# Kernel optimization log

Measured on AMD Instinct MI355X. Metric: run time of the kernel, lower is better.

Reference implementation:

```python
import jax, jax.numpy as jnp
import numpy as np

GRID = np.array([128, 128, 128], dtype=np.int32)
CENTER = np.array([0.0, 0.0, 0.0], dtype=np.float32)
SIZE = np.array([200.0, 200.0, 200.0], dtype=np.float32)
KERNEL_WIDTH = 3.0
TOF_BIN = 1.0
TOF_SIGMA2 = 100.0
N_SAMPLES = 64  # samples per LOR
N_LORS = 100000


def _ray_points_weights(lors):
    # lors: [N,7] = (x1,y1,z1, x2,y2,z2, tof)
    p1, p2, tof = lors[:, :3], lors[:, 3:6], lors[:, 6]
    u = (jnp.arange(N_SAMPLES, dtype=lors.dtype) + 0.5) / N_SAMPLES  # [S]
    pts = p1[:, None, :] + u[None, :, None] * (p2 - p1)[:, None, :]  # [N,S,3]
    L = jnp.linalg.norm(p2 - p1, axis=-1)  # [N]
    d = (u[None, :] - 0.5) * L[:, None]    # signed distance from LOR midpoint [N,S]
    tc = (tof * TOF_BIN)[:, None]          # TOF-estimated annihilation offset
    gauss = jnp.exp(-0.5 * (d - tc) ** 2 / TOF_SIGMA2)
    w = gauss * (L / N_SAMPLES)[:, None] * KERNEL_WIDTH  # [N,S]
    return pts, w


def _trilinear_corners(pts, grid, center, size):
    g = jnp.asarray(np.asarray(grid, np.int32))
    gf = g.astype(pts.dtype)
    c = jnp.asarray(np.asarray(center, np.float32), pts.dtype)
    s = jnp.asarray(np.asarray(size, np.float32), pts.dtype)
    vox = (pts - (c - s / 2)) / (s / gf) - 0.5  # continuous voxel coords [N,S,3]
    i0 = jnp.floor(vox).astype(jnp.int32)
    f = vox - i0.astype(pts.dtype)
    corners = []
    for dx in (0, 1):
        for dy in (0, 1):
            for dz in (0, 1):
                off = jnp.array([dx, dy, dz], jnp.int32)
                ii = i0 + off
                wxyz = jnp.where(off == 1, f, 1 - f)  # [N,S,3]
                w = wxyz[..., 0] * wxyz[..., 1] * wxyz[..., 2]
                inb = jnp.all((ii >= 0) & (ii < g), axis=-1)
                iic = jnp.clip(ii, 0, g - 1)
                corners.append((iic, jnp.where(inb, w, jnp.zeros_like(w))))
    return corners


def projection(lors, image, grid, center, size):
    pts, w = _ray_points_weights(lors)
    vals = jnp.zeros(w.shape, w.dtype)
    for ii, cw in _trilinear_corners(pts, grid, center, size):
        vals = vals + cw * image[ii[..., 0], ii[..., 1], ii[..., 2]]
    return jnp.sum(vals * w, axis=1)  # [N]


def backprojection(lors, lor_values, grid, center, size, dtype):
    pts, w = _ray_points_weights(lors)
    contrib = lor_values[:, None] * w  # [N,S]
    g = tuple(int(x) for x in np.asarray(grid))
    strides = (g[1] * g[2], g[2], 1)
    flat = jnp.zeros(g[0] * g[1] * g[2], dtype)
    for ii, cw in _trilinear_corners(pts, grid, center, size):
        idx = ii[..., 0] * strides[0] + ii[..., 1] * strides[1] + ii[..., 2]
        flat = flat.at[idx.ravel()].add((contrib * cw).ravel())
    return flat.reshape(g)


def setup_inputs() -> dict:
    key = jax.random.key(0)
    k_img, k_eff, kx, ky, kz = jax.random.split(key, 5)
    shape = tuple(int(x) for x in GRID)
    image = jax.random.uniform(k_img, shape, dtype=jnp.float32)
    efficiency_map = jax.random.uniform(k_eff, shape, dtype=jnp.float32) + 0.5

    def make_lors(k):
        k1, k2 = jax.random.split(k)
        ends = jax.random.uniform(k1, (6, N_LORS), minval=-100.0, maxval=100.0)
        tof = jax.random.uniform(k2, (1, N_LORS), minval=-30.0, maxval=30.0)
        return jnp.concatenate([ends, tof], axis=0).astype(jnp.float32)  # [7,N]

    return {
        "image": image,
        "efficiency_map": efficiency_map,
        "xlors": make_lors(kx),
        "ylors": make_lors(ky),
        "zlors": make_lors(kz),
    }


def reference(image, efficiency_map, xlors, ylors, zlors):
    imgz = jnp.transpose(image)             # reverse axes, as tf.transpose
    imgx = jnp.transpose(imgz, (2, 0, 1))
    imgy = jnp.transpose(imgz, (1, 0, 2))
    effmap = jnp.transpose(efficiency_map)
    xl, yl, zl = xlors.T, ylors.T, zlors.T  # [N,7]

    # z-view
    pz = projection(zl, imgz, GRID, CENTER, SIZE)
    bpz = backprojection(zl, pz, GRID, CENTER, SIZE, image.dtype)

    # x-view: permute axes [0,2,1]
    gx, cx, sx = GRID[[0, 2, 1]], CENTER[[0, 2, 1]], SIZE[[0, 2, 1]]
    px = projection(xl, imgx, gx, cx, sx)
    bpx = backprojection(xl, px, gx, cx, sx, image.dtype)
    bpxt = jnp.transpose(bpx, (1, 2, 0))

    # y-view: permute axes [1,2,0]
    gy, cy, sy = GRID[[1, 2, 0]], CENTER[[1, 2, 0]], SIZE[[1, 2, 0]]
    py = projection(yl, imgy, gy, cy, sy)
    bpy = backprojection(yl, py, gy, cy, sy, image.dtype)
    bpyt = jnp.transpose(bpy, (1, 0, 2))

    result = imgz / effmap * (bpxt + bpyt + bpz)
    return jnp.transpose(result)
```

## Files before the change

### kernel.cpp

```cpp
#include <hip/hip_runtime.h>

#define NLOR 100000
#define NDL  300000
#define NS   64
#define G    128
#define NVOX (G*G*G)
#define EPS_A 0.05f
#define W_MIN 1.5e-4f
#define NBKT   256
#define NSLICE 16
#define HALO_N 9537
#define ACC17  4913
#define MAX_SLOTS 1024
#define REC_CAP 19200000u
#define QSCALE     32768.0f
#define INV_QSCALE (1.0f/32768.0f)

typedef unsigned int u32;
typedef unsigned long long u64;

#define O_COUNTS  0ull
#define O_OFF     32768ull
#define O_CURSOR  65536ull
#define O_SLOTOFF 98304ull
#define O_SLOT2Q  102400ull
#define O_RECS    131072ull
#define O_COPIES  (O_RECS + (u64)REC_CAP * 8ull)
#define WS_NEED   (O_COPIES + (u64)MAX_SLOTS * HALO_N * 4ull)

__device__ __forceinline__ void atomAddF32(float* p, float v) { unsafeAtomicAdd(p, v); }

struct Samp { float w, fA, fB, fC; int iA, iB, iC; };

__device__ __forceinline__ Samp sample_abc(const float* __restrict__ lp,
                                           int lor, int dir, int lane)
{
    const float p10 = lp[0 * NLOR + lor];
    const float p11 = lp[1 * NLOR + lor];
    const float p12 = lp[2 * NLOR + lor];
    const float d0  = lp[3 * NLOR + lor] - p10;
    const float d1  = lp[4 * NLOR + lor] - p11;
    const float d2  = lp[5 * NLOR + lor] - p12;
    const float tof = lp[6 * NLOR + lor];

    const float L = sqrtf(d0 * d0 + d1 * d1 + d2 * d2);
    const float u = ((float)lane + 0.5f) * (1.0f / NS);
    const float dd = (u - 0.5f) * L - tof;
    const float w = __expf(dd * dd * (-0.5f / 100.0f)) * L * (3.0f / NS);

    const float inv_vs = 1.0f / 1.5625f;
    const float v0 = (p10 + u * d0 + 100.0f) * inv_vs - 0.5f;
    const float v1 = (p11 + u * d1 + 100.0f) * inv_vs - 0.5f;
    const float v2 = (p12 + u * d2 + 100.0f) * inv_vs - 0.5f;

    const float f0 = floorf(v0), f1 = floorf(v1), f2 = floorf(v2);
    const int i0 = (int)f0, i1 = (int)f1, i2 = (int)f2;
    const float g0 = v0 - f0, g1 = v1 - f1, g2 = v2 - f2;

    Samp s; s.w = w;
    if (dir == 0)      { s.iA = i0; s.fA = g0; s.iB = i2; s.fB = g2; s.iC = i1; s.fC = g1; }
    else if (dir == 1) { s.iA = i2; s.fA = g2; s.iB = i0; s.fB = g0; s.iC = i1; s.fC = g1; }
    else               { s.iA = i2; s.fA = g2; s.iB = i1; s.fB = g1; s.iC = i0; s.fC = g0; }
    return s;
}

__device__ __forceinline__ int bucket_of(const Samp& s) {
    const int qA = (s.iA < 0 ? 0 : s.iA) >> 4;
    const int qB = (s.iB < 0 ? 0 : s.iB) >> 4;
    const int qC = (s.iC < 0 ? 0 : s.iC) >> 5;
    return (qA << 5) | (qB << 2) | qC;
}

__device__ __forceinline__ u64 encode_rec(const Samp& s, float sc) {
    const u32 qfA = min((int)(s.fA * 512.0f + 0.5f), 511);
    const u32 qfB = min((int)(s.fB * 512.0f + 0.5f), 511);
    const u32 qfC = min((int)(s.fC * 512.0f + 0.5f), 511);
    const u32 s13 = (__float_as_uint(sc) + 0x40000u) >> 19;
    return (u64)qfA | ((u64)qfB << 9) | ((u64)qfC << 18)
         | ((u64)(u32)(s.iA + 1) << 27) | ((u64)(u32)(s.iB + 1) << 35)
         | ((u64)(u32)(s.iC + 1) << 43) | ((u64)s13 << 51);
}

struct RunInfo { bool leader; int runlen; int ldr; };

__device__ __forceinline__ RunInfo run_detect(bool act, int q, int lane) {
    RunInfo r;
    const u64 act_mask = __ballot(act);
    const int qup = __shfl_up(q, 1, 64);
    r.leader = act && (lane == 0 || !((act_mask >> (lane - 1)) & 1ull) || qup != q);
    const u64 lead_mask = __ballot(r.leader);
    r.runlen = 0;
    if (r.leader) {
        const u64 stop_mask = (~act_mask) | lead_mask;
        const u64 gt = (lane == 63) ? 0ull : (stop_mask >> (lane + 1));
        const int e = gt ? (lane + 1 + (__ffsll((unsigned long long)gt) - 1)) : 64;
        r.runlen = e - lane;
    }
    r.ldr = 0;
    if (act) {
        const u64 below_eq = lead_mask &
            ((lane == 63) ? ~0ull : ((1ull << (lane + 1)) - 1ull));
        r.ldr = 63 - __clzll((unsigned long long)below_eq);
    }
    return r;
}

__global__ __launch_bounds__(256) void count_kernel(
    const float* __restrict__ xl, const float* __restrict__ yl, const float* __restrict__ zl,
    u32* __restrict__ counts)
{
    __shared__ u32 h[NBKT];
    const int tid = (int)threadIdx.x;
    h[tid] = 0;
    __syncthreads();
    const int wid = tid >> 6, lane = tid & 63;
    const int slice = (int)blockIdx.x & (NSLICE - 1);

    for (int dl = (int)blockIdx.x * 4 + wid; dl < NDL; dl += 8192) {
        const int dir = dl < NLOR ? 0 : (dl < 2 * NLOR ? 1 : 2);
        const int lor = dl - dir * NLOR;
        const float* lp = dir == 0 ? xl : (dir == 1 ? yl : zl);
        const Samp s = sample_abc(lp, lor, dir, lane);
        const bool act_w = (s.w >= W_MIN);
        const int q = bucket_of(s);
        const RunInfo r = run_detect(act_w, q, lane);
        if (r.leader) atomicAdd(&h[q], (u32)r.runlen);
    }
    __syncthreads();
    if (h[tid]) atomicAdd(&counts[tid * NSLICE + slice], h[tid]);
}

__global__ __launch_bounds__(1024) void scan_kernel(
    const u32* __restrict__ counts, u32* __restrict__ off, u32* __restrict__ cursor,
    u32* __restrict__ slot_off, u32* __restrict__ slot2q)
{
    __shared__ u32 part[1024];
    __shared__ u32 sl[256];
    const int t = (int)threadIdx.x;
    u32 c[4], ssum = 0;
    #pragma unroll
    for (int k = 0; k < 4; ++k) { c[k] = counts[t * 4 + k]; ssum += c[k]; }
    part[t] = ssum;
    __syncthreads();
    for (int ofs = 1; ofs < 1024; ofs <<= 1) {
        u32 v = (t >= ofs) ? part[t - ofs] : 0u;
        __syncthreads();
        part[t] += v;
        __syncthreads();
    }
    u32 run = (t == 0) ? 0u : part[t - 1];
    #pragma unroll
    for (int k = 0; k < 4; ++k) { off[t * 4 + k] = run; cursor[t * 4 + k] = run; run += c[k]; }
    if (t == 1023) off[4096] = part[1023];
    __syncthreads();

    if (t < 256) {
        const u32 len = part[t * 4 + 3] - (t ? part[t * 4 - 1] : 0u);
        const u32 total = part[1023];
        u32 target = (total + 699u) / 700u;
        if (target == 0) target = 1;
        u32 slots = (len + target - 1u) / target;
        slots = slots < 1u ? 1u : (slots > 64u ? 64u : slots);
        sl[t] = slots;
    }
    __syncthreads();
    for (int ofs = 1; ofs < 256; ofs <<= 1) {
        u32 v = (t >= ofs && t < 256) ? sl[t - ofs] : 0u;
        __syncthreads();
        if (t < 256) sl[t] += v;
        __syncthreads();
    }
    if (t < 256) {
        const u32 base = t ? sl[t - 1] : 0u;
        const u32 n = sl[t] - base;
        slot_off[t] = base;
        for (u32 k = 0; k < n; ++k) slot2q[base + k] = (u32)t;
        if (t == 255) slot_off[256] = sl[255];
    }
}

__global__ __launch_bounds__(256) void projscat_kernel(
    const float* __restrict__ img,
    const float* __restrict__ xl, const float* __restrict__ yl, const float* __restrict__ zl,
    const u32* __restrict__ off, u32* __restrict__ cursor, u64* __restrict__ recs)
{
    const int tid = (int)threadIdx.x;
    const int wid = tid >> 6, lane = tid & 63;
    const int slice = (int)blockIdx.x & (NSLICE - 1);

    for (int dl = (int)blockIdx.x * 4 + wid; dl < NDL; dl += 8192) {
        const int dir = dl < NLOR ? 0 : (dl < 2 * NLOR ? 1 : 2);
        const int lor = dl - dir * NLOR;
        const float* lp = dir == 0 ? xl : (dir == 1 ? yl : zl);
        const Samp s = sample_abc(lp, lor, dir, lane);

        float val = 0.0f;
        if (s.w >= W_MIN) {
            const float wA1 = s.fA, wA0 = 1.0f - s.fA;
            const float wB1 = s.fB, wB0 = 1.0f - s.fB;
            const float wC1 = s.fC, wC0 = 1.0f - s.fC;
            #pragma unroll
            for (int c = 0; c < 8; ++c) {
                const int oA = (c >> 2) & 1, oB = (c >> 1) & 1, oC = c & 1;
                const int A = s.iA + oA, B = s.iB + oB, C = s.iC + oC;
                const bool ok = ((unsigned)A < 128u) & ((unsigned)B < 128u) & ((unsigned)C < 128u);
                const int Ac = min(max(A, 0), 127), Bc = min(max(B, 0), 127), Cc = min(max(C, 0), 127);
                const float cw = ok ? (oA ? wA1 : wA0) * (oB ? wB1 : wB0) * (oC ? wC1 : wC0) : 0.0f;
                val += cw * img[(Ac << 14) | (Bc << 7) | Cc];
            }
        }
        float lv = val * s.w;
        #pragma unroll
        for (int off2 = 32; off2 > 0; off2 >>= 1) lv += __shfl_xor(lv, off2, 64);
        const float sc = lv * s.w;

        const bool act = (s.w >= W_MIN) && (sc >= EPS_A);
        const int q = bucket_of(s);
        const RunInfo r = run_detect(act, q, lane);
        u32 base = 0, bound = 0;
        if (r.leader) {
            base  = atomicAdd(&cursor[q * NSLICE + slice], (u32)r.runlen);
            bound = off[q * NSLICE + slice + 1];
        }
        if (act) {
            const u64 rec = encode_rec(s, sc);
            const u32 mybase  = (u32)__shfl((int)base,  r.ldr, 64);
            const u32 mybound = (u32)__shfl((int)bound, r.ldr, 64);
            const u32 idx = mybase + (u32)(lane - r.ldr);
            if (idx < mybound) recs[idx] = rec;
        }
    }
}

__global__ __launch_bounds__(512) void bproj_bucket(
    const u64* __restrict__ recs, const u32* __restrict__ off,
    const u32* __restrict__ cursor,
    const u32* __restrict__ slot_off, const u32* __restrict__ slot2q,
    float* __restrict__ copies)
{
    __shared__ u64 acc[ACC17];
    const int s = (int)blockIdx.x;
    if ((u32)s >= slot_off[256]) return;
    const int tid = (int)threadIdx.x;
    const int q = (int)slot2q[s];
    const u32 so = slot_off[q], so1 = slot_off[q + 1];
    const u32 k = (u32)s - so, n = so1 - so;

    for (int i = tid; i < ACC17; i += 512) acc[i] = 0ull;
    __syncthreads();

    const int baseA = (q >> 5) << 4, baseB = ((q >> 2) & 7) << 4, baseC = (q & 3) << 5;

    for (int sl = 0; sl < NSLICE; ++sl) {
        const u32 lo  = off[q * NSLICE + sl];
        const u32 hiW = cursor[q * NSLICE + sl];
        for (u32 i = lo + k * 512u + (u32)tid; i < hiW; i += n * 512u) {
            const u64 v = recs[i];
            const float fA = (float)(v & 511) * (1.0f / 512.0f);
            const float fB = (float)((v >> 9) & 511) * (1.0f / 512.0f);
            const float fC = (float)((v >> 18) & 511) * (1.0f / 512.0f);
            const int lA0 = (int)((v >> 27) & 255) - 1 - baseA;
            const int lB0 = (int)((v >> 35) & 255) - 1 - baseB;
            const int lC0 = (int)((v >> 43) & 255) - 1 - baseC;
            const float sc = __uint_as_float((u32)(v >> 51) << 19);
            const float wC0 = (1.0f - fC) * sc, wC1 = fC * sc;
            const int lc1 = lC0 + 1;
            const bool c0in = (lC0 >= 0);
            const bool c1in = (baseC + lc1 <= 127);
            #pragma unroll
            for (int ab = 0; ab < 4; ++ab) {
                const int oA = ab & 1, oB = ab >> 1;
                const int la = lA0 + oA, lb = lB0 + oB;
                const bool okab = (la >= 0) & (lb >= 0) &
                                  (baseA + la <= 127) & (baseB + lb <= 127);
                const float wab = (oA ? fA : 1.0f - fA) * (oB ? fB : 1.0f - fB);
                const float w0 = wC0 * wab, w1 = wC1 * wab;
                const u32 q0 = (okab & c0in && w0 >= EPS_A) ? (u32)(w0 * QSCALE + 0.5f) : 0u;
                const u32 q1 = (okab & c1in && w1 >= EPS_A) ? (u32)(w1 * QSCALE + 0.5f) : 0u;
                if (q0 | q1) {
                    const int rowbase = (la * 17 + lb) * 17;
                    if (lC0 >= 0 && !(lC0 & 1)) {
                        atomicAdd(&acc[rowbase + (lC0 >> 1)], (u64)q0 | ((u64)q1 << 32));
                    } else {
                        if (q0) atomicAdd(&acc[rowbase + (lC0 >> 1)], (u64)q0 << 32);
                        if (q1) atomicAdd(&acc[rowbase + (lc1 >> 1)], (u64)q1);
                    }
                }
            }
        }
    }
    __syncthreads();

    float* dst = copies + (size_t)s * HALO_N;
    for (int i = tid; i < HALO_N; i += 512) {
        const int la = i / 561;
        const int rem = i - la * 561;
        const int lb = rem / 33;
        const int lc = rem - lb * 33;
        const u64 wv = acc[(la * 17 + lb) * 17 + (lc >> 1)];
        const u32 hv = (lc & 1) ? (u32)(wv >> 32) : (u32)wv;
        dst[i] = (float)hv * INV_QSCALE;
    }
}

__global__ __launch_bounds__(256) void finalize_halo(
    const float* __restrict__ img, const float* __restrict__ eff,
    const float* __restrict__ copies, const u32* __restrict__ slot_off,
    float* __restrict__ out)
{
    const int i = (int)blockIdx.x * 256 + (int)threadIdx.x;
    const int A = i >> 14, B = (i >> 7) & 127, C = i & 127;
    const int qA = A >> 4, la = A & 15;
    const int qB = B >> 4, lb = B & 15;
    const int qC = C >> 5, lc = C & 31;
    float S = 0.0f;
    #pragma unroll
    for (int d = 0; d < 8; ++d) {
        const int dA = d & 1, dB = (d >> 1) & 1, dC = (d >> 2) & 1;
        if (dA && (la != 0 || qA == 0)) continue;
        if (dB && (lb != 0 || qB == 0)) continue;
        if (dC && (lc != 0 || qC == 0)) continue;
        const int sq = ((qA - dA) << 5) | ((qB - dB) << 2) | (qC - dC);
        const int sla = dA ? 16 : la, slb = dB ? 16 : lb, slc = dC ? 32 : lc;
        const int lidx = (sla * 17 + slb) * 33 + slc;
        const u32 s0 = slot_off[sq], s1 = slot_off[sq + 1];
        for (u32 s = s0; s < s1; ++s) S += copies[(size_t)s * HALO_N + lidx];
    }
    out[i] = img[i] / eff[i] * S;
}

__global__ __launch_bounds__(256) void tor_direct(const float* __restrict__ img,
                                                  const float* __restrict__ lors,
                                                  int dir, float* __restrict__ acc)
{
    const int gid = (int)blockIdx.x * 256 + (int)threadIdx.x;
    const int lor = gid >> 6, lane = (int)threadIdx.x & 63;
    if (lor >= NLOR) return;
    const Samp s = sample_abc(lors, lor, dir, lane);
    const bool active = (s.w >= W_MIN);
    float val = 0.0f;
    int   fl[8]; float cw8[8];
    if (active) {
        const float wA1 = s.fA, wA0 = 1.0f - s.fA;
        const float wB1 = s.fB, wB0 = 1.0f - s.fB;
        const float wC1 = s.fC, wC0 = 1.0f - s.fC;
        #pragma unroll
        for (int c = 0; c < 8; ++c) {
            const int oA = (c >> 2) & 1, oB = (c >> 1) & 1, oC = c & 1;
            const int A = s.iA + oA, B = s.iB + oB, Cv = s.iC + oC;
            const bool ok = ((unsigned)A < 128u) & ((unsigned)B < 128u) & ((unsigned)Cv < 128u);
            const int Ac = min(max(A, 0), 127), Bc = min(max(B, 0), 127), Cc = min(max(Cv, 0), 127);
            const float cw = ok ? (oA ? wA1 : wA0) * (oB ? wB1 : wB0) * (oC ? wC1 : wC0) : 0.0f;
            fl[c] = (Ac << 14) | (Bc << 7) | Cc; cw8[c] = cw;
            val += cw * img[fl[c]];
        }
    }
    float lv = val * s.w;
    #pragma unroll
    for (int off = 32; off > 0; off >>= 1) lv += __shfl_xor(lv, off, 64);
    if (!active) return;
    const float sc = lv * s.w;
    #pragma unroll
    for (int c = 0; c < 8; ++c) {
        const float a = sc * cw8[c];
        if (a >= EPS_A) atomAddF32(&acc[fl[c]], a);
    }
}

__global__ __launch_bounds__(256) void finalize_f32(const float* __restrict__ img,
                                                    const float* __restrict__ eff,
                                                    float* __restrict__ out)
{
    const int i = (int)blockIdx.x * 256 + (int)threadIdx.x;
    out[i] = img[i] / eff[i] * out[i];
}

extern "C" void kernel_launch(void* const* d_in, const int* in_sizes, int n_in,
                              void* d_out, int out_size, void* d_ws, size_t ws_size,
                              hipStream_t stream) {
    const float* img = (const float*)d_in[0];
    const float* eff = (const float*)d_in[1];
    const float* xl  = (const float*)d_in[2];
    const float* yl  = (const float*)d_in[3];
    const float* zl  = (const float*)d_in[4];
    float* out = (float*)d_out;
    char* ws = (char*)d_ws;

    if (ws_size >= WS_NEED) {
        u32*   counts  = (u32*)(ws + O_COUNTS);
        u32*   off     = (u32*)(ws + O_OFF);
        u32*   cursor  = (u32*)(ws + O_CURSOR);
        u32*   sloto   = (u32*)(ws + O_SLOTOFF);
        u32*   slot2q  = (u32*)(ws + O_SLOT2Q);
        u64*   recs    = (u64*)(ws + O_RECS);
        float* copies  = (float*)(ws + O_COPIES);

        hipMemsetAsync(counts, 0, 4096 * sizeof(u32), stream);

        count_kernel<<<2048, 256, 0, stream>>>(xl, yl, zl, counts);
        scan_kernel<<<1, 1024, 0, stream>>>(counts, off, cursor, sloto, slot2q);
        projscat_kernel<<<2048, 256, 0, stream>>>(img, xl, yl, zl, off, cursor, recs);
        bproj_bucket<<<MAX_SLOTS, 512, 0, stream>>>(recs, off, cursor, sloto, slot2q, copies);
        finalize_halo<<<NVOX / 256, 256, 0, stream>>>(img, eff, copies, sloto, out);
    } else {
        hipMemsetAsync(out, 0, (size_t)NVOX * sizeof(float), stream);
        const dim3 blk(256), grd((NLOR * NS) / 256);
        tor_direct<<<grd, blk, 0, stream>>>(img, xl, 0, out);
        tor_direct<<<grd, blk, 0, stream>>>(img, yl, 1, out);
        tor_direct<<<grd, blk, 0, stream>>>(img, zl, 2, out);
        finalize_f32<<<NVOX / 256, 256, 0, stream>>>(img, eff, out);
    }
}
```

Measured before the change: 528.4 us.

## Sort LORs by TOF-center tile and assign contiguous chunks per XCD

Adds a counting-sort pre-pass that bins each LOR by the 16^3 tile containing its TOF-weighted centre, then writes axis-permuted LOR parameters into a packed 8-float array in tile order. The count and projection kernels read this sorted array and give each XCD-interleaved block group one contiguous chunk. The goal is better L2 locality for image gathers and for record-bucket atomics. The change also lowers MAX_SLOTS to 768 and the per-slot target divisor to 512, and adds three small kernels plus a roughly 10 MB intermediate buffer.

```diff
diff --git a/kernel.cpp b/kernel.cpp
--- a/kernel.cpp
+++ b/kernel.cpp
@@ -11,7 +11,7 @@
 #define NSLICE 16
 #define HALO_N 9537
 #define ACC17  4913
-#define MAX_SLOTS 1024
+#define MAX_SLOTS 768
 #define REC_CAP 19200000u
 #define QSCALE     32768.0f
 #define INV_QSCALE (1.0f/32768.0f)
@@ -24,7 +24,11 @@
 #define O_CURSOR  65536ull
 #define O_SLOTOFF 98304ull
 #define O_SLOT2Q  102400ull
-#define O_RECS    131072ull
+#define O_TCNT    106496ull
+#define O_TOFF    110592ull
+#define O_TCUR    114688ull
+#define O_PARAMS  131072ull
+#define O_RECS    9764864ull
 #define O_COPIES  (O_RECS + (u64)REC_CAP * 8ull)
 #define WS_NEED   (O_COPIES + (u64)MAX_SLOTS * HALO_N * 4ull)
 
@@ -32,8 +36,9 @@
 
 struct Samp { float w, fA, fB, fC; int iA, iB, iC; };
 
-__device__ __forceinline__ Samp sample_abc(const float* __restrict__ lp,
-                                           int lor, int dir, int lane)
+__device__ __forceinline__ void load_map(const float* __restrict__ lp, int lor, int dir,
+                                         float& p1A, float& p1B, float& p1C,
+                                         float& dA, float& dB, float& dC, float& tof)
 {
     const float p10 = lp[0 * NLOR + lor];
     const float p11 = lp[1 * NLOR + lor];
@@ -41,27 +46,39 @@
     const float d0  = lp[3 * NLOR + lor] - p10;
     const float d1  = lp[4 * NLOR + lor] - p11;
     const float d2  = lp[5 * NLOR + lor] - p12;
-    const float tof = lp[6 * NLOR + lor];
-
-    const float L = sqrtf(d0 * d0 + d1 * d1 + d2 * d2);
+    tof = lp[6 * NLOR + lor];
+    if (dir == 0)      { p1A = p10; dA = d0; p1B = p12; dB = d2; p1C = p11; dC = d1; }
+    else if (dir == 1) { p1A = p12; dA = d2; p1B = p10; dB = d0; p1C = p11; dC = d1; }
+    else               { p1A = p12; dA = d2; p1B = p11; dB = d1; p1C = p10; dC = d0; }
+}
+
+__device__ __forceinline__ Samp samp_from(float p1A, float p1B, float p1C,
+                                          float dA, float dB, float dC,
+                                          float tof, int lane)
+{
+    const float L = sqrtf(dA * dA + dB * dB + dC * dC);
     const float u = ((float)lane + 0.5f) * (1.0f / NS);
     const float dd = (u - 0.5f) * L - tof;
     const float w = __expf(dd * dd * (-0.5f / 100.0f)) * L * (3.0f / NS);
 
     const float inv_vs = 1.0f / 1.5625f;
-    const float v0 = (p10 + u * d0 + 100.0f) * inv_vs - 0.5f;
-    const float v1 = (p11 + u * d1 + 100.0f) * inv_vs - 0.5f;
-    const float v2 = (p12 + u * d2 + 100.0f) * inv_vs - 0.5f;
-
-    const float f0 = floorf(v0), f1 = floorf(v1), f2 = floorf(v2);
-    const int i0 = (int)f0, i1 = (int)f1, i2 = (int)f2;
-    const float g0 = v0 - f0, g1 = v1 - f1, g2 = v2 - f2;
-
+    const float vA = (p1A + u * dA + 100.0f) * inv_vs - 0.5f;
+    const float vB = (p1B + u * dB + 100.0f) * inv_vs - 0.5f;
+    const float vC = (p1C + u * dC + 100.0f) * inv_vs - 0.5f;
+
+    const float fa = floorf(vA), fb = floorf(vB), fc = floorf(vC);
     Samp s; s.w = w;
-    if (dir == 0)      { s.iA = i0; s.fA = g0; s.iB = i2; s.fB = g2; s.iC = i1; s.fC = g1; }
-    else if (dir == 1) { s.iA = i2; s.fA = g2; s.iB = i0; s.fB = g0; s.iC = i1; s.fC = g1; }
-    else               { s.iA = i2; s.fA = g2; s.iB = i1; s.fB = g1; s.iC = i0; s.fC = g0; }
+    s.iA = (int)fa; s.iB = (int)fb; s.iC = (int)fc;
+    s.fA = vA - fa; s.fB = vB - fb; s.fC = vC - fc;
     return s;
+}
+
+__device__ __forceinline__ Samp sample_abc(const float* __restrict__ lp,
+                                           int lor, int dir, int lane)
+{
+    float p1A, p1B, p1C, dA, dB, dC, tof;
+    load_map(lp, lor, dir, p1A, p1B, p1C, dA, dB, dC, tof);
+    return samp_from(p1A, p1B, p1C, dA, dB, dC, tof, lane);
 }
 
 __device__ __forceinline__ int bucket_of(const Samp& s) {
@@ -105,9 +122,73 @@
     return r;
 }
 
+__device__ __forceinline__ int center_tile(const float* __restrict__ lp, int lor, int dir) {
+    float p1A, p1B, p1C, dA, dB, dC, tof;
+    load_map(lp, lor, dir, p1A, p1B, p1C, dA, dB, dC, tof);
+    const float L = sqrtf(dA * dA + dB * dB + dC * dC);
+    float uc = 0.5f + (L > 0.0f ? tof / L : 0.0f);
+    uc = fminf(fmaxf(uc, 0.0f), 1.0f);
+    const float inv_vs = 1.0f / 1.5625f;
+    const float cA = (p1A + uc * dA + 100.0f) * inv_vs - 0.5f;
+    const float cB = (p1B + uc * dB + 100.0f) * inv_vs - 0.5f;
+    const float cC = (p1C + uc * dC + 100.0f) * inv_vs - 0.5f;
+    const int tA = min(max((int)floorf(cA * (1.0f / 16.0f)), 0), 7);
+    const int tB = min(max((int)floorf(cB * (1.0f / 16.0f)), 0), 7);
+    const int tC = min(max((int)floorf(cC * (1.0f / 16.0f)), 0), 7);
+    return (tA << 6) | (tB << 3) | tC;
+}
+
+__global__ __launch_bounds__(256) void lor_prep(
+    const float* __restrict__ xl, const float* __restrict__ yl, const float* __restrict__ zl,
+    u32* __restrict__ tcnt)
+{
+    const int dl = (int)blockIdx.x * 256 + (int)threadIdx.x;
+    if (dl >= NDL) return;
+    const int dir = dl < NLOR ? 0 : (dl < 2 * NLOR ? 1 : 2);
+    const int lor = dl - dir * NLOR;
+    const float* lp = dir == 0 ? xl : (dir == 1 ? yl : zl);
+    atomicAdd(&tcnt[center_tile(lp, lor, dir)], 1u);
+}
+
+__global__ __launch_bounds__(512) void scan512(
+    const u32* __restrict__ tcnt, u32* __restrict__ toff, u32* __restrict__ tcur)
+{
+    __shared__ u32 p[512];
+    const int t = (int)threadIdx.x;
+    p[t] = tcnt[t];
+    __syncthreads();
+    for (int ofs = 1; ofs < 512; ofs <<= 1) {
+        u32 v = (t >= ofs) ? p[t - ofs] : 0u;
+        __syncthreads();
+        p[t] += v;
+        __syncthreads();
+    }
+    const u32 excl = t ? p[t - 1] : 0u;
+    toff[t] = excl; tcur[t] = excl;
+    if (t == 511) toff[512] = p[511];
+}
+
+__global__ __launch_bounds__(256) void lor_place(
+    const float* __restrict__ xl, const float* __restrict__ yl, const float* __restrict__ zl,
+    u32* __restrict__ tcur, float* __restrict__ params)
+{
+    const int dl = (int)blockIdx.x * 256 + (int)threadIdx.x;
+    if (dl >= NDL) return;
+    const int dir = dl < NLOR ? 0 : (dl < 2 * NLOR ? 1 : 2);
+    const int lor = dl - dir * NLOR;
+    const float* lp = dir == 0 ? xl : (dir == 1 ? yl : zl);
+    float p1A, p1B, p1C, dA, dB, dC, tof;
+    load_map(lp, lor, dir, p1A, p1B, p1C, dA, dB, dC, tof);
+    const int key = center_tile(lp, lor, dir);
+    const u32 pos = atomicAdd(&tcur[key], 1u);
+    float* dst = params + (size_t)pos * 8;
+    dst[0] = p1A; dst[1] = p1B; dst[2] = p1C;
+    dst[3] = dA;  dst[4] = dB;  dst[5] = dC;
+    dst[6] = tof; dst[7] = 0.0f;
+}
+
 __global__ __launch_bounds__(256) void count_kernel(
-    const float* __restrict__ xl, const float* __restrict__ yl, const float* __restrict__ zl,
-    u32* __restrict__ counts)
+    const float* __restrict__ params, u32* __restrict__ counts)
 {
     __shared__ u32 h[NBKT];
     const int tid = (int)threadIdx.x;
@@ -115,12 +196,14 @@
     __syncthreads();
     const int wid = tid >> 6, lane = tid & 63;
     const int slice = (int)blockIdx.x & (NSLICE - 1);
-
-    for (int dl = (int)blockIdx.x * 4 + wid; dl < NDL; dl += 8192) {
-        const int dir = dl < NLOR ? 0 : (dl < 2 * NLOR ? 1 : 2);
-        const int lor = dl - dir * NLOR;
-        const float* lp = dir == 0 ? xl : (dir == 1 ? yl : zl);
-        const Samp s = sample_abc(lp, lor, dir, lane);
+    const int xcd = (int)blockIdx.x & 7;
+    const int sub = (int)blockIdx.x >> 3;
+    const int CH = NDL / 8;
+    const int base = xcd * CH;
+
+    for (int j = sub * 4 + wid; j < CH; j += 1024) {
+        const float* pk = params + (size_t)(base + j) * 8;
+        const Samp s = samp_from(pk[0], pk[1], pk[2], pk[3], pk[4], pk[5], pk[6], lane);
         const bool act_w = (s.w >= W_MIN);
         const int q = bucket_of(s);
         const RunInfo r = run_detect(act_w, q, lane);
@@ -157,7 +240,7 @@
     if (t < 256) {
         const u32 len = part[t * 4 + 3] - (t ? part[t * 4 - 1] : 0u);
         const u32 total = part[1023];
-        u32 target = (total + 699u) / 700u;
+        u32 target = (total + 511u) / 512u;
         if (target == 0) target = 1;
         u32 slots = (len + target - 1u) / target;
         slots = slots < 1u ? 1u : (slots > 64u ? 64u : slots);
@@ -180,19 +263,20 @@
 }
 
 __global__ __launch_bounds__(256) void projscat_kernel(
-    const float* __restrict__ img,
-    const float* __restrict__ xl, const float* __restrict__ yl, const float* __restrict__ zl,
+    const float* __restrict__ img, const float* __restrict__ params,
     const u32* __restrict__ off, u32* __restrict__ cursor, u64* __restrict__ recs)
 {
     const int tid = (int)threadIdx.x;
     const int wid = tid >> 6, lane = tid & 63;
     const int slice = (int)blockIdx.x & (NSLICE - 1);
-
-    for (int dl = (int)blockIdx.x * 4 + wid; dl < NDL; dl += 8192) {
-        const int dir = dl < NLOR ? 0 : (dl < 2 * NLOR ? 1 : 2);
-        const int lor = dl - dir * NLOR;
-        const float* lp = dir == 0 ? xl : (dir == 1 ? yl : zl);
-        const Samp s = sample_abc(lp, lor, dir, lane);
+    const int xcd = (int)blockIdx.x & 7;
+    const int sub = (int)blockIdx.x >> 3;
+    const int CH = NDL / 8;
+    const int base = xcd * CH;
+
+    for (int j = sub * 4 + wid; j < CH; j += 1024) {
+        const float* pk = params + (size_t)(base + j) * 8;
+        const Samp s = samp_from(pk[0], pk[1], pk[2], pk[3], pk[4], pk[5], pk[6], lane);
 
         float val = 0.0f;
         if (s.w >= W_MIN) {
@@ -217,14 +301,14 @@
         const bool act = (s.w >= W_MIN) && (sc >= EPS_A);
         const int q = bucket_of(s);
         const RunInfo r = run_detect(act, q, lane);
-        u32 base = 0, bound = 0;
+        u32 rbase = 0, bound = 0;
         if (r.leader) {
-            base  = atomicAdd(&cursor[q * NSLICE + slice], (u32)r.runlen);
+            rbase = atomicAdd(&cursor[q * NSLICE + slice], (u32)r.runlen);
             bound = off[q * NSLICE + slice + 1];
         }
         if (act) {
             const u64 rec = encode_rec(s, sc);
-            const u32 mybase  = (u32)__shfl((int)base,  r.ldr, 64);
+            const u32 mybase  = (u32)__shfl((int)rbase, r.ldr, 64);
             const u32 mybound = (u32)__shfl((int)bound, r.ldr, 64);
             const u32 idx = mybase + (u32)(lane - r.ldr);
             if (idx < mybound) recs[idx] = rec;
@@ -392,14 +476,21 @@
         u32*   cursor  = (u32*)(ws + O_CURSOR);
         u32*   sloto   = (u32*)(ws + O_SLOTOFF);
         u32*   slot2q  = (u32*)(ws + O_SLOT2Q);
+        u32*   tcnt    = (u32*)(ws + O_TCNT);
+        u32*   toff    = (u32*)(ws + O_TOFF);
+        u32*   tcur    = (u32*)(ws + O_TCUR);
+        float* params  = (float*)(ws + O_PARAMS);
         u64*   recs    = (u64*)(ws + O_RECS);
         float* copies  = (float*)(ws + O_COPIES);
 
-        hipMemsetAsync(counts, 0, 4096 * sizeof(u32), stream);
-
-        count_kernel<<<2048, 256, 0, stream>>>(xl, yl, zl, counts);
+        hipMemsetAsync(ws, 0, 116736, stream);
+
+        lor_prep<<<(NDL + 255) / 256, 256, 0, stream>>>(xl, yl, zl, tcnt);
+        scan512<<<1, 512, 0, stream>>>(tcnt, toff, tcur);
+        lor_place<<<(NDL + 255) / 256, 256, 0, stream>>>(xl, yl, zl, tcur, params);
+        count_kernel<<<2048, 256, 0, stream>>>(params, counts);
         scan_kernel<<<1, 1024, 0, stream>>>(counts, off, cursor, sloto, slot2q);
-        projscat_kernel<<<2048, 256, 0, stream>>>(img, xl, yl, zl, off, cursor, recs);
+        projscat_kernel<<<2048, 256, 0, stream>>>(img, params, off, cursor, recs);
         bproj_bucket<<<MAX_SLOTS, 512, 0, stream>>>(recs, off, cursor, sloto, slot2q, copies);
         finalize_halo<<<NVOX / 256, 256, 0, stream>>>(img, eff, copies, sloto, out);
     } else {
```

After: 800.6 us. 1.52x slower.
